# Kernel tuning notes

Measured on AMD Instinct MI355X. Metric: run time of the kernel, lower is better.

Reference implementation:

```python
import jax, jax.numpy as jnp
import numpy as np

N = 4096      # num nodes
E = 131072    # num edges
D = 128       # embed dim (in=out)
HID = 16      # kan hidden dim
G, K = 4, 3   # KAN grid_size / spline_order (GCN + FFN kans)
GA, KA = 2, 1 # attention KANLinear grid_size / spline_order
H, HD = 8, 16 # heads, head_dim

def make_grid(in_f, g, k):
    h = 2.0 / g
    pts = (np.arange(-k, g + k + 1) * h - 1.0).astype(np.float32)  # [g+2k+1]
    return jnp.asarray(np.tile(pts[None, :], (in_f, 1)))            # [in_f, g+2k+1]

GRID_D = make_grid(D, G, K)
GRID_H = make_grid(HID, G, K)
GRID_A = make_grid(D, GA, KA)

def b_splines(x, grid, k):
    # x: [n, in] -> B-spline bases [n, in, g+k] via Cox-de-Boor recursion
    x = x[:, :, None]
    g = grid[None]
    bases = ((x >= g[..., :-1]) & (x < g[..., 1:])).astype(x.dtype)
    for j in range(1, k + 1):
        bases = ((x - g[..., :-(j + 1)]) / (g[..., j:-1] - g[..., :-(j + 1)]) * bases[..., :-1]
                 + (g[..., j + 1:] - x) / (g[..., j + 1:] - g[..., 1:-j]) * bases[..., 1:])
    return bases

def kan_lin(x, bw, sw, grid, k, use_silu):
    base = jax.nn.silu(x) if use_silu else x
    return base @ bw.T + jnp.einsum('nig,oig->no', b_splines(x, grid, k), sw)

def ekan2(x, bw1, sw1, bw2, sw2):
    # eKAN with layers_hidden=[D, HID, D], SiLU base activation
    h = kan_lin(x, bw1, sw1, GRID_D, K, True)
    return kan_lin(h, bw2, sw2, GRID_H, K, True)

def layer_norm(h, s, b):
    m = jnp.mean(h, axis=-1, keepdims=True)
    v = jnp.var(h, axis=-1, keepdims=True)
    return (h - m) * jax.lax.rsqrt(v + 1e-5) * s + b

def setup_inputs() -> dict:
    key = jax.random.key(0)
    ks = jax.random.split(key, 20)
    r = lambda i, shape: jax.random.normal(ks[i], shape, jnp.float32) * 0.1
    return dict(
        x=jax.random.normal(ks[0], (N, D), jnp.float32),
        edge_index=jax.random.randint(ks[1], (2, E), 0, N),
        gcn_bw1=r(2, (HID, D)), gcn_sw1=r(3, (HID, D, G + K)),
        gcn_bw2=r(4, (D, HID)), gcn_sw2=r(5, (D, HID, G + K)),
        q_bw=r(6, (D, D)), q_sw=r(7, (D, D, GA + KA)),
        k_bw=r(8, (D, D)), k_sw=r(9, (D, D, GA + KA)),
        v_bw=r(10, (D, D)), v_sw=r(11, (D, D, GA + KA)),
        ffn_bw1=r(12, (HID, D)), ffn_sw1=r(13, (HID, D, G + K)),
        ffn_bw2=r(14, (D, HID)), ffn_sw2=r(15, (D, HID, G + K)),
        ln1_s=jnp.ones(D), ln1_b=jnp.zeros(D),
        ln2_s=jnp.ones(D), ln2_b=jnp.zeros(D),
        ln3_s=jnp.ones(D), ln3_b=jnp.zeros(D),
    )

def reference(x, edge_index, gcn_bw1, gcn_sw1, gcn_bw2, gcn_sw2,
              q_bw, q_sw, k_bw, k_sw, v_bw, v_sw,
              ffn_bw1, ffn_sw1, ffn_bw2, ffn_sw2,
              ln1_s, ln1_b, ln2_s, ln2_b, ln3_s, ln3_b):
    n = x.shape[0]
    # ---- local GCN-KAN branch: KAN(A_hat x) ----
    loops = jnp.arange(n)
    row = jnp.concatenate([edge_index[0], loops])  # sources (+ self-loops)
    col = jnp.concatenate([edge_index[1], loops])  # targets
    w = jnp.ones(row.shape[0], x.dtype)
    deg = jax.ops.segment_sum(w, row, num_segments=n)
    dis = jnp.where(deg > 0, deg ** -0.5, 0.0)
    norm = dis[row] * w * dis[col]
    agg = jax.ops.segment_sum(norm[:, None] * x[row], col, num_segments=n)  # [n, D]
    h_local = ekan2(agg, gcn_bw1, gcn_sw1, gcn_bw2, gcn_sw2)
    h_local = layer_norm(x + h_local, ln1_s, ln1_b)
    # ---- global KAN multi-head attention branch ----
    Q = kan_lin(x, q_bw, q_sw, GRID_A, KA, False).reshape(n, H, HD)
    Kv = kan_lin(x, k_bw, k_sw, GRID_A, KA, False).reshape(n, H, HD)
    V = kan_lin(x, v_bw, v_sw, GRID_A, KA, False).reshape(n, H, HD)
    scores = jnp.einsum('nhd,mhd->hnm', Q, Kv) / np.sqrt(HD)  # [H, n, n]
    attn = jax.nn.softmax(scores, axis=-1)
    h_attn = jnp.einsum('hnm,mhd->nhd', attn, V).reshape(n, D)
    h_attn = layer_norm(x + h_attn, ln2_s, ln2_b)
    # ---- combine + KAN feed-forward ----
    h = h_local + h_attn
    out = layer_norm(h + ekan2(h, ffn_bw1, ffn_sw1, ffn_bw2, ffn_sw2), ln3_s, ln3_b)
    return out
```

## Files before the change

### kernel.cpp

```cpp
#include <hip/hip_runtime.h>

typedef unsigned short u16;
typedef unsigned int u32;

#define D_ 128
#define HID_ 16
#define NH_ 8
#define HD_ 16
#define PSTRIDE 17

#define WE_W1G 0
#define WE_W2G 16384
#define WE_W1F 32768
#define WE_W2F 49152
#define WE_TOTAL 65536

#define KROW 24
#define VROW 136
#define PROW 40
#define HROW 136

#define QSCALE 0.3606737602222409f

typedef __attribute__((ext_vector_type(8))) short bfrag;
typedef __attribute__((ext_vector_type(4))) float ffrag;

#if defined(__has_builtin)
#if __has_builtin(__builtin_amdgcn_exp2f)
#define EXP2F(x) __builtin_amdgcn_exp2f(x)
#endif
#endif
#ifndef EXP2F
#define EXP2F(x) exp2f(x)
#endif


__device__ __forceinline__ float bf2f(u16 u) {
    union { u32 i; float f; } v; v.i = ((u32)u) << 16; return v.f;
}
__device__ __forceinline__ u16 f2bf(float f) {
    u32 x = __float_as_uint(f);
    u32 r = (x + 0x7fffu + ((x >> 16) & 1u)) >> 16;
    return (u16)r;
}
__device__ __forceinline__ float rdf(const void* p, int i, bool bf) {
    return bf ? bf2f(((const u16*)p)[i]) : ((const float*)p)[i];
}

__global__ __launch_bounds__(256) void k_detect(const void* x,
                         const void* gbw1, const void* gsw1, const void* gbw2, const void* gsw2,
                         const void* qbw, const void* qsw, const void* kbw, const void* ksw,
                         const void* vbw, const void* vsw,
                         const void* fbw1, const void* fsw1, const void* fbw2, const void* fsw2,
// ... 143 lines not shown
    for (int k = 0; k < 4; k++) a[k] = (base + k < N) ? cnt[base + k] : 0;
    int loc = a[0] + a[1] + a[2] + a[3];
    int pre = loc;
#pragma unroll
    for (int off = 1; off < 64; off <<= 1) {
        int v = __shfl_up(pre, off, 64);
        if ((t & 63) >= off) pre += v;
    }
    if ((t & 63) == 63) ws[t >> 6] = pre;
    __syncthreads();
    if (t < 64) {
        int v = (t < 16) ? ws[t] : 0;
#pragma unroll
        for (int off = 1; off < 16; off <<= 1) {
            int u = __shfl_up(v, off, 64);
            if (t >= off) v += u;
        }
        if (t < 16) ws[t] = v;
    }
    __syncthreads();
    int ex = pre - loc + ((t >= 64) ? ws[(t >> 6) - 1] : 0);
    int run = ex;
#pragma unroll
    for (int k = 0; k < 4; k++) {
        if (base + k < N) rowptr[base + k] = run;
        run += a[k];
    }
    if (t == 1023) rowptr[N] = ws[15];
#pragma unroll
    for (int k = 0; k < 4; k++)
        if (base + k < N) dis[base + k] = rsqrtf((float)degi[base + k] + 1.0f);
}

__global__ void k_fill(const int* __restrict__ ei, const int* __restrict__ rowptr,
                       int* __restrict__ fill, int* __restrict__ elist, int E) {
    int e = blockIdx.x * 256 + threadIdx.x;
    if (e < E) {
        int r = ei[e], c = ei[E + e];
        int pos = rowptr[c] + atomicAdd(&fill[c], 1);
        elist[pos] = r;
    }
}

__global__ __launch_bounds__(128) void k_gcn(const int* __restrict__ rowptr,
        const int* __restrict__ elist, const float* __restrict__ dis,
        const float* __restrict__ xin, u16* __restrict__ Afeat) {
    int c = blockIdx.x, t = threadIdx.x;
    __shared__ int ids[128];
    __shared__ float wsh[128];
    int beg = rowptr[c], end = rowptr[c + 1];
    float a0 = 0.0f, a1 = 0.0f, a2 = 0.0f, a3 = 0.0f;
    for (int j0 = beg; j0 < end; j0 += 128) {
        int cc = min(128, end - j0);
        __syncthreads();
        if (t < cc) {
            int rr = elist[j0 + t];
            ids[t] = rr;
            wsh[t] = dis[rr];
        }
        __syncthreads();
        int j = 0;
        for (; j + 4 <= cc; j += 4) {
            a0 += wsh[j]     * xin[(size_t)ids[j]     * D_ + t];
            a1 += wsh[j + 1] * xin[(size_t)ids[j + 1] * D_ + t];
            a2 += wsh[j + 2] * xin[(size_t)ids[j + 2] * D_ + t];
            a3 += wsh[j + 3] * xin[(size_t)ids[j + 3] * D_ + t];
        }
        for (; j < cc; j++) a0 += wsh[j] * xin[(size_t)ids[j] * D_ + t];
    }
    float dc = dis[c];
    float a = dc * (((a0 + a1) + (a2 + a3)) + dc * xin[(size_t)c * D_ + t]);
    ((uint4*)Afeat)[(size_t)c * D_ + t] = feat8(a);
}

#define EKAN_G1_4W(APTR, ASTR, W1B) { \
    const u16* ar = (APTR) + (size_t)l15 * (ASTR) + (size_t)ww * 256 + quad * 8; \
    const u16* br = (W1B) + (size_t)l15 * 1024 + (size_t)ww * 256 + quad * 8; \
    ffrag c0 = {0,0,0,0}, c1 = {0,0,0,0}; \
    for (int ks = 0; ks < 128; ks += 32) { \
        c0 = __builtin_amdgcn_mfma_f32_16x16x32_bf16(*(const bfrag*)(ar + ks),       *(const bfrag*)(br + ks),       c0, 0, 0, 0); \
        c1 = __builtin_amdgcn_mfma_f32_16x16x32_bf16(*(const bfrag*)(ar + 128 + ks), *(const bfrag*)(br + 128 + ks), c1, 0, 0, 0); \
    } \
    redG[ww][lane] = make_float4(c0.x + c1.x, c0.y + c1.y, c0.z + c1.z, c0.w + c1.w); \
    __syncthreads(); \
    if (ww == 0) { \
        float4 p0 = redG[0][lane], p1 = redG[1][lane], p2 = redG[2][lane], p3 = redG[3][lane]; \
        float e0 = (p0.x + p1.x) + (p2.x + p3.x); \
        float e1 = (p0.y + p1.y) + (p2.y + p3.y); \
        float e2 = (p0.z + p1.z) + (p2.z + p3.z); \
        float e3 = (p0.w + p1.w) + (p2.w + p3.w); \
        { uint4 fv = feat8(e0); *(uint4*)(&hfL[(quad * 4 + 0) * HROW + l15 * 8]) = fv; } \
        { uint4 fv = feat8(e1); *(uint4*)(&hfL[(quad * 4 + 1) * HROW + l15 * 8]) = fv; } \
        { uint4 fv = feat8(e2); *(uint4*)(&hfL[(quad * 4 + 2) * HROW + l15 * 8]) = fv; } \
        { uint4 fv = feat8(e3); *(uint4*)(&hfL[(quad * 4 + 3) * HROW + l15 * 8]) = fv; } \
    } }

#define EK_TGET(RR, COMP, V0, V1, RES0EXPR, RES1EXPR) { \
    int row = quad * 4 + RR; \
    float r0 = (RES0EXPR); \
    float r1 = (RES1EXPR); \
    V0 = a0.COMP + r0; V1 = a1.COMP + r1; \
    float s1 = V0 + V1, s2 = V0 * V0 + V1 * V1; \
    s1 += __shfl_xor(s1, 1, 64); s2 += __shfl_xor(s2, 1, 64); \
    s1 += __shfl_xor(s1, 2, 64); s2 += __shfl_xor(s2, 2, 64); \
    s1 += __shfl_xor(s1, 4, 64); s2 += __shfl_xor(s2, 4, 64); \
// ... 29 lines not shown
    int c0i = 32 * ww + l15, c1i = c0i + 16; \
    float ls0 = (LNS)[c0i], lb0 = (LNB)[c0i]; \
    float ls1 = (LNS)[c1i], lb1 = (LNB)[c1i]; \
    float v0r0, v0r1, v0r2, v0r3, v1r0, v1r1, v1r2, v1r3; \
    EK_TGET(0, x, v0r0, v1r0, RES0EXPR, RES1EXPR) \
    EK_TGET(1, y, v0r1, v1r1, RES0EXPR, RES1EXPR) \
    EK_TGET(2, z, v0r2, v1r2, RES0EXPR, RES1EXPR) \
    EK_TGET(3, w, v0r3, v1r3, RES0EXPR, RES1EXPR) \
    __syncthreads(); \
    EK_TOUT(0, v0r0, v1r0, OUTP, BFO) \
    EK_TOUT(1, v0r1, v1r1, OUTP, BFO) \
    EK_TOUT(2, v0r2, v1r2, OUTP, BFO) \
    EK_TOUT(3, v0r3, v1r3, OUTP, BFO) }

__global__ __launch_bounds__(256) void k_ekan4(const u16* __restrict__ A,
        const u16* __restrict__ W1b, const u16* __restrict__ W2b,
        const float* __restrict__ resid,
        const float* __restrict__ lns, const float* __restrict__ lnb,
        void* __restrict__ outp, const u32* __restrict__ flags, int fin, int N) {
    __shared__ u16 hfL[16 * HROW];
    __shared__ float redS[128];
    __shared__ float4 redG[4][64];
    int mt = blockIdx.x, t = threadIdx.x;
    int ww = t >> 6, lane = t & 63, quad = lane >> 4, l15 = lane & 15;
    int node0 = mt * 16;
    const u16* Ab = A + (size_t)node0 * 1024;
    bool bfo = (fin != 0) && (flags[0] != 0);
    EKAN_G1_4W(Ab, 1024, W1b)
    __syncthreads();
    EKAN_G2LN(W2b, lns, lnb,
              resid[(size_t)(node0 + row) * 128 + c0i],
              resid[(size_t)(node0 + row) * 128 + c1i],
              outp, bfo)
}

#define QKV_STORE(ACC, TL) { \
    int col = cg * 48 + (TL) * 16 + l15; \
    int mat = col >> 7, idx = col & 127; \
    u16* dstb = (mat == 0) ? Qb : (mat == 1) ? Kb : Vb; \
    size_t base = (size_t)(idx >> 4) * N * HD_ + (size_t)(idx & 15); \
    dstb[base + (size_t)(rowb + 0) * HD_] = f2bf(ACC.x); \
    dstb[base + (size_t)(rowb + 1) * HD_] = f2bf(ACC.y); \
    dstb[base + (size_t)(rowb + 2) * HD_] = f2bf(ACC.z); \
    dstb[base + (size_t)(rowb + 3) * HD_] = f2bf(ACC.w); \
}

__global__ __launch_bounds__(64) void k_qkv5(const u16* __restrict__ F,
        const u16* __restrict__ Wb,
        u16* __restrict__ Qb, u16* __restrict__ Kb, u16* __restrict__ Vb, int N) {
    int mt = blockIdx.x, cg = blockIdx.y;
    int lane = threadIdx.x, quad = lane >> 4, l15 = lane & 15;
    const u16* arow = F + (size_t)(mt * 16 + l15) * 512 + quad * 8;
    const u16* b0r = Wb + (size_t)(cg * 48 + l15) * 512 + quad * 8;
    const u16* b1r = b0r + 16 * 512;
    const u16* b2r = b0r + 32 * 512;
    ffrag a0 = {0, 0, 0, 0}, a1 = {0, 0, 0, 0}, a2 = {0, 0, 0, 0};
#pragma unroll
    for (int ks = 0; ks < 512; ks += 32) {
        bfrag af = *(const bfrag*)(arow + ks);
        bfrag bf0 = *(const bfrag*)(b0r + ks);
        bfrag bf1 = *(const bfrag*)(b1r + ks);
        bfrag bf2 = *(const bfrag*)(b2r + ks);
        a0 = __builtin_amdgcn_mfma_f32_16x16x32_bf16(af, bf0, a0, 0, 0, 0);
        a1 = __builtin_amdgcn_mfma_f32_16x16x32_bf16(af, bf1, a1, 0, 0, 0);
        a2 = __builtin_amdgcn_mfma_f32_16x16x32_bf16(af, bf2, a2, 0, 0, 0);
    }
    int rowb = mt * 16 + quad * 4;
    QKV_STORE(a0, 0)
    QKV_STORE(a1, 1)
    QKV_STORE(a2, 2)
}

#define ATTN_SCORE(QF, LACC, PBT) { \
    ffrag zz = {0.0f, 0.0f, 0.0f, 0.0f}; \
    ffrag s0 = __builtin_amdgcn_mfma_f32_16x16x32_bf16(QF, kf0, zz, 0, 0, 0); \
    ffrag s1 = __builtin_amdgcn_mfma_f32_16x16x32_bf16(QF, kf1, zz, 0, 0, 0); \
    float a0 = EXP2F(s0.x), a1 = EXP2F(s0.y), a2 = EXP2F(s0.z), a3 = EXP2F(s0.w); \
    float b0 = EXP2F(s1.x), b1 = EXP2F(s1.y), b2 = EXP2F(s1.z), b3 = EXP2F(s1.w); \
    LACC.x += a0 + b0; LACC.y += a1 + b1; LACC.z += a2 + b2; LACC.w += a3 + b3; \
    u32* pw = (u32*)PBT; \
    pw[(quad * 4 + 0) * (PROW / 2) + l15] = (__float_as_uint(a0) >> 16) | (__float_as_uint(b0) & 0xFFFF0000u); \
    pw[(quad * 4 + 1) * (PROW / 2) + l15] = (__float_as_uint(a1) >> 16) | (__float_as_uint(b1) & 0xFFFF0000u); \
    pw[(quad * 4 + 2) * (PROW / 2) + l15] = (__float_as_uint(a2) >> 16) | (__float_as_uint(b2) & 0xFFFF0000u); \
    pw[(quad * 4 + 3) * (PROW / 2) + l15] = (__float_as_uint(a3) >> 16) | (__float_as_uint(b3) & 0xFFFF0000u); \
}

#define ATTN_PV(OACC, PBT) { \
    bfrag pf = *(const bfrag*)(&PBT[l15 * PROW + quad * 8]); \
    OACC = __builtin_amdgcn_mfma_f32_16x16x32_bf16(pf, vf, OACC, 0, 0, 0); \
}

#define STORE_TILE(OACC, LACC, TL) { \
    int q0 = qtb + (TL) * 16 + quad * 4; \
    float* pp; \
    pp = part + ((size_t)(h * N + q0 + 0) * SPLIT + s) * PSTRIDE; \
    pp[1 + l15] = OACC.x; if (l15 == 0) pp[0] = LACC.x; \
    pp = part + ((size_t)(h * N + q0 + 1) * SPLIT + s) * PSTRIDE; \
    pp[1 + l15] = OACC.y; if (l15 == 0) pp[0] = LACC.y; \
    pp = part + ((size_t)(h * N + q0 + 2) * SPLIT + s) * PSTRIDE; \
    pp[1 + l15] = OACC.z; if (l15 == 0) pp[0] = LACC.z; \
    pp = part + ((size_t)(h * N + q0 + 3) * SPLIT + s) * PSTRIDE; \
    pp[1 + l15] = OACC.w; if (l15 == 0) pp[0] = LACC.w; \
}

__global__ __launch_bounds__(256) void k_attn9(const u16* __restrict__ Qb,
        const u16* __restrict__ Kb, const u16* __restrict__ Vb,
        float* __restrict__ part, int N, int SPLIT) {
    int s = blockIdx.x, qb = blockIdx.y, h = blockIdx.z;
    int t = threadIdx.x;
    int w = t >> 6, lane = t & 63, quad = lane >> 4, l15 = lane & 15;
    __shared__ u16 ldsK[128 * KROW + 16];
    __shared__ u16 ldsVt[16 * VROW];
    __shared__ u16 ldsP[4][4][16 * PROW];

    const u16* qrow = Qb + (size_t)h * N * HD_;
    const u16* krow = Kb + (size_t)h * N * HD_;
    const u16* vrow = Vb + (size_t)h * N * HD_;

    for (int i = t; i < (128 * KROW + 16) / 2; i += 256) ((u32*)ldsK)[i] = 0;

    int qtb = qb * 256 + w * 64;
    bfrag qz = {0, 0, 0, 0, 0, 0, 0, 0};
    bfrag qf0 = qz, qf1 = qz, qf2 = qz, qf3 = qz;
    if (quad < 2) {
        qf0 = *(const bfrag*)(qrow + (size_t)(qtb + 0 * 16 + l15) * HD_ + quad * 8);
        qf1 = *(const bfrag*)(qrow + (size_t)(qtb + 1 * 16 + l15) * HD_ + quad * 8);
        qf2 = *(const bfrag*)(qrow + (size_t)(qtb + 2 * 16 + l15) * HD_ + quad * 8);
        qf3 = *(const bfrag*)(qrow + (size_t)(qtb + 3 * 16 + l15) * HD_ + quad * 8);
    }

    ffrag o0 = {0, 0, 0, 0}, o1 = {0, 0, 0, 0}, o2 = {0, 0, 0, 0}, o3 = {0, 0, 0, 0};
    ffrag L0 = {0, 0, 0, 0}, L1 = {0, 0, 0, 0}, L2 = {0, 0, 0, 0}, L3 = {0, 0, 0, 0};
    u16* pb0 = &ldsP[w][0][0];
    u16* pb1 = &ldsP[w][1][0];
    u16* pb2 = &ldsP[w][2][0];
    u16* pb3 = &ldsP[w][3][0];

    int keys = N / SPLIT;
    int kstart0 = s * keys;
    for (int kst = 0; kst < keys; kst += 128) {
        int kg = kstart0 + kst;
        __syncthreads();
        if (t < 128) {
            const uint4* src = (const uint4*)(krow + (size_t)(kg + t) * HD_);
            uint4 a = src[0], b = src[1];
            *(uint4*)(&ldsK[t * KROW]) = a;
            *(uint4*)(&ldsK[t * KROW + 8]) = b;
        } else {
            int key = t - 128;
            const uint4* src = (const uint4*)(vrow + (size_t)(kg + key) * HD_);
            uint4 a = src[0], b = src[1];
            ldsVt[0 * VROW + key] = (u16)(a.x);  ldsVt[1 * VROW + key] = (u16)(a.x >> 16);
            ldsVt[2 * VROW + key] = (u16)(a.y);  ldsVt[3 * VROW + key] = (u16)(a.y >> 16);
            ldsVt[4 * VROW + key] = (u16)(a.z);  ldsVt[5 * VROW + key] = (u16)(a.z >> 16);
            ldsVt[6 * VROW + key] = (u16)(a.w);  ldsVt[7 * VROW + key] = (u16)(a.w >> 16);
            ldsVt[8 * VROW + key] = (u16)(b.x);  ldsVt[9 * VROW + key] = (u16)(b.x >> 16);
            ldsVt[10 * VROW + key] = (u16)(b.y); ldsVt[11 * VROW + key] = (u16)(b.y >> 16);
            ldsVt[12 * VROW + key] = (u16)(b.z); ldsVt[13 * VROW + key] = (u16)(b.z >> 16);
            ldsVt[14 * VROW + key] = (u16)(b.w); ldsVt[15 * VROW + key] = (u16)(b.w >> 16);
        }
        __syncthreads();
#pragma unroll
        for (int koff = 0; koff < 128; koff += 32) {
            bfrag kf0 = *(const bfrag*)(&ldsK[(koff + 2 * l15) * KROW + quad * 8]);
            bfrag kf1 = *(const bfrag*)(&ldsK[(koff + 2 * l15 + 1) * KROW + quad * 8]);
            bfrag vf = *(const bfrag*)(&ldsVt[l15 * VROW + koff + quad * 8]);
            ATTN_SCORE(qf0, L0, pb0)
            ATTN_SCORE(qf1, L1, pb1)
            ATTN_SCORE(qf2, L2, pb2)
            ATTN_SCORE(qf3, L3, pb3)
            __asm__ volatile("s_waitcnt lgkmcnt(0)" ::: "memory");
            ATTN_PV(o0, pb0)
            ATTN_PV(o1, pb1)
            ATTN_PV(o2, pb2)
            ATTN_PV(o3, pb3)
        }
    }

#pragma unroll
    for (int off = 1; off < 16; off <<= 1) {
        L0.x += __shfl_xor(L0.x, off, 64); L0.y += __shfl_xor(L0.y, off, 64);
        L0.z += __shfl_xor(L0.z, off, 64); L0.w += __shfl_xor(L0.w, off, 64);
        L1.x += __shfl_xor(L1.x, off, 64); L1.y += __shfl_xor(L1.y, off, 64);
        L1.z += __shfl_xor(L1.z, off, 64); L1.w += __shfl_xor(L1.w, off, 64);
        L2.x += __shfl_xor(L2.x, off, 64); L2.y += __shfl_xor(L2.y, off, 64);
        L2.z += __shfl_xor(L2.z, off, 64); L2.w += __shfl_xor(L2.w, off, 64);
        L3.x += __shfl_xor(L3.x, off, 64); L3.y += __shfl_xor(L3.y, off, 64);
        L3.z += __shfl_xor(L3.z, off, 64); L3.w += __shfl_xor(L3.w, off, 64);
    }
    STORE_TILE(o0, L0, 0)
    STORE_TILE(o1, L1, 1)
    STORE_TILE(o2, L2, 2)
    STORE_TILE(o3, L3, 3)
}

__global__ __launch_bounds__(128) void k_comb(const float* __restrict__ part,
        const float* __restrict__ xin, const float* __restrict__ hl,
        const float* __restrict__ lnp, float* __restrict__ hv,
        u16* __restrict__ Afeat, int N, int SPLIT) {
    int n = blockIdx.x, t = threadIdx.x;
    __shared__ float red[128];
    int h = t >> 4, d = t & 15;
    float L = 0.0f, O = 0.0f;
    for (int ss = 0; ss < SPLIT; ss++) {
        const float* ps = part + ((size_t)(h * N + n) * SPLIT + ss) * PSTRIDE;
        L += ps[0];
        O += ps[1 + d];
    }
    float ha = O / L;
    float r = xin[(size_t)n * D_ + t] + ha;
    float mean = bsum(r, red) * (1.0f / 128.0f);
    float c = r - mean;
    float var = bsum(c * c, red) * (1.0f / 128.0f);
    float y2 = c * rsqrtf(var + 1e-5f) * lnp[256 + t] + lnp[384 + t];
    float hvv = hl[(size_t)n * D_ + t] + y2;
    hv[(size_t)n * D_ + t] = hvv;
    ((uint4*)Afeat)[(size_t)n * D_ + t] = feat8(hvv);
}

extern "C" void kernel_launch(void* const* d_in, const int* in_sizes, int n_in,
                              void* d_out, int out_size, void* d_ws, size_t ws_size,
                              hipStream_t stream) {
    const void* x = d_in[0];
    const int* ei = (const int*)d_in[1];
    const void* gbw1 = d_in[2];
    const void* gsw1 = d_in[3];
// ... 19 lines not shown
    const int N = in_sizes[0] / D_;
    const int E = in_sizes[1] / 2;
    const size_t ND = (size_t)N * D_;

    float* wf = (float*)d_ws;
    u32* flags = (u32*)wf;
    float* lnp = wf + 32;
    float* dis = wf + 800;
    float* xin = dis + N;
    float* hl  = xin + ND;
    float* hv  = hl + ND;
    u16* Web = (u16*)(hv + ND);
    u16* Wb  = Web + WE_TOTAL;
    u16* F   = Wb + 196608;
    u16* Qb  = F + (size_t)N * 512;
    u16* Kb  = Qb + ND;
    u16* Vb  = Kb + ND;
    u16* Afeat = Vb + ND;
    int* cnt    = (int*)(Afeat + (size_t)N * 1024);
    int* fill   = cnt + N;
    int* degi   = fill + N;
    int* rowptr = degi + N;
    int* elist  = rowptr + N + 1;
    float* part = (float*)(elist + E);

    size_t baseBytes = (size_t)((char*)part - (char*)d_ws);
    int SPLIT = 8;
    if (baseBytes + (size_t)NH_ * N * 8 * PSTRIDE * 4 > ws_size) SPLIT = 4;
    if (baseBytes + (size_t)NH_ * N * 4 * PSTRIDE * 4 > ws_size) SPLIT = 2;

    int convB = ((N * D_ + 768) + 255) >> 8;
    int countB = (E + 255) / 256;
    int zeroB = (3 * N + 255) / 256;

    k_detect<<<21 + zeroB, 256, 0, stream>>>(x, gbw1, gsw1, gbw2, gsw2, qbw, qsw, kbw, ksw,
                                             vbw, vsw, fbw1, fsw1, fbw2, fsw2,
                                             ln1s, ln1b, ln2s, ln2b, ln3s, ln3b, flags, cnt, N);
    k_setup<<<convB + 224 + countB, 256, 0, stream>>>(
        x, ln1s, ln1b, ln2s, ln2b, ln3s, ln3b,
        gbw1, gsw1, gbw2, gsw2, fbw1, fsw1, fbw2, fsw2,
        qbw, qsw, kbw, ksw, vbw, vsw,
        ei, flags, xin, lnp, F, Web, Wb, cnt, degi, N, E);
    k_qkv5<<<dim3(N / 16, 8), 64, 0, stream>>>(F, Wb, Qb, Kb, Vb, N);
    k_scan<<<1, 1024, 0, stream>>>(cnt, degi, rowptr, dis, N);
    k_fill<<<countB, 256, 0, stream>>>(ei, rowptr, fill, elist, E);
    k_gcn<<<N, 128, 0, stream>>>(rowptr, elist, dis, xin, Afeat);
    k_ekan4<<<N / 16, 256, 0, stream>>>(Afeat, Web + WE_W1G, Web + WE_W2G, xin,
                                        lnp + 0, lnp + 128, hl, flags, 0, N);
    k_attn9<<<dim3(SPLIT, N / 256, NH_), 256, 0, stream>>>(Qb, Kb, Vb, part, N, SPLIT);
    k_comb<<<N, 128, 0, stream>>>(part, xin, hl, lnp, hv, Afeat, N, SPLIT);
    k_ekan4<<<N / 16, 256, 0, stream>>>(Afeat, Web + WE_W1F, Web + WE_W2F, hv,
                                        lnp + 512, lnp + 640, d_out, flags, 1, N);
}
```

Baseline: 233.7 us.

## Co-schedule independent kernels: fuse QKV with edge fill, attention with GCN

Merges independent stages into shared launches by splitting the grid: the QKV projection blocks run alongside the CSR edge-fill blocks, and the attention blocks run alongside the GCN aggregation blocks, which now handle two nodes per 256-thread block. This removes two kernel launches and lets the memory-bound gather and atomics overlap with the MFMA-heavy attention. The cost is heterogeneous blocks sharing one LDS allocation and launch bound, and the eKAN GCN stage must now wait for attention to finish before it starts.

```diff
diff --git a/kernel.cpp b/kernel.cpp
--- a/kernel.cpp
+++ b/kernel.cpp
@@ -19,6 +19,13 @@
 #define VROW 136
 #define PROW 40
 #define HROW 136
+
+#define SH_K 0
+#define SH_KN (128 * KROW + 16)
+#define SH_VT (SH_KN)
+#define SH_VTN (16 * VROW)
+#define SH_P (SH_KN + SH_VTN)
+#define SH_TOTAL (SH_P + 16 * 16 * PROW)
 
 #define QSCALE 0.3606737602222409f
 
@@ -228,45 +235,223 @@
         if (base + k < N) dis[base + k] = rsqrtf((float)degi[base + k] + 1.0f);
 }
 
-__global__ void k_fill(const int* __restrict__ ei, const int* __restrict__ rowptr,
-                       int* __restrict__ fill, int* __restrict__ elist, int E) {
-    int e = blockIdx.x * 256 + threadIdx.x;
-    if (e < E) {
-        int r = ei[e], c = ei[E + e];
-        int pos = rowptr[c] + atomicAdd(&fill[c], 1);
-        elist[pos] = r;
-    }
-}
-
-__global__ __launch_bounds__(128) void k_gcn(const int* __restrict__ rowptr,
-        const int* __restrict__ elist, const float* __restrict__ dis,
-        const float* __restrict__ xin, u16* __restrict__ Afeat) {
-    int c = blockIdx.x, t = threadIdx.x;
-    __shared__ int ids[128];
-    __shared__ float wsh[128];
-    int beg = rowptr[c], end = rowptr[c + 1];
-    float a0 = 0.0f, a1 = 0.0f, a2 = 0.0f, a3 = 0.0f;
-    for (int j0 = beg; j0 < end; j0 += 128) {
-        int cc = min(128, end - j0);
-        __syncthreads();
-        if (t < cc) {
-            int rr = elist[j0 + t];
-            ids[t] = rr;
-            wsh[t] = dis[rr];
-        }
-        __syncthreads();
-        int j = 0;
-        for (; j + 4 <= cc; j += 4) {
-            a0 += wsh[j]     * xin[(size_t)ids[j]     * D_ + t];
-            a1 += wsh[j + 1] * xin[(size_t)ids[j + 1] * D_ + t];
-            a2 += wsh[j + 2] * xin[(size_t)ids[j + 2] * D_ + t];
-            a3 += wsh[j + 3] * xin[(size_t)ids[j + 3] * D_ + t];
-        }
-        for (; j < cc; j++) a0 += wsh[j] * xin[(size_t)ids[j] * D_ + t];
-    }
-    float dc = dis[c];
-    float a = dc * (((a0 + a1) + (a2 + a3)) + dc * xin[(size_t)c * D_ + t]);
-    ((uint4*)Afeat)[(size_t)c * D_ + t] = feat8(a);
+#define QKV_STORE(ACC, TL) { \
+    int col = cg * 48 + (TL) * 16 + l15; \
+    int mat = col >> 7, idx = col & 127; \
+    u16* dstb = (mat == 0) ? Qb : (mat == 1) ? Kb : Vb; \
+    size_t base = (size_t)(idx >> 4) * N * HD_ + (size_t)(idx & 15); \
+    dstb[base + (size_t)(rowb + 0) * HD_] = f2bf(ACC.x); \
+    dstb[base + (size_t)(rowb + 1) * HD_] = f2bf(ACC.y); \
+    dstb[base + (size_t)(rowb + 2) * HD_] = f2bf(ACC.z); \
+    dstb[base + (size_t)(rowb + 3) * HD_] = f2bf(ACC.w); \
+}
+
+__global__ __launch_bounds__(256) void k_qkv_fill(const u16* __restrict__ F,
+        const u16* __restrict__ Wb,
+        u16* __restrict__ Qb, u16* __restrict__ Kb, u16* __restrict__ Vb,
+        const int* __restrict__ ei, const int* __restrict__ rowptr,
+        int* __restrict__ fill, int* __restrict__ elist, int N, int E) {
+    int b = blockIdx.x, t = threadIdx.x;
+    int qkvB = (N / 16) * 2;
+    if (b < qkvB) {
+        int sub = b * 4 + (t >> 6);
+        int mt = sub >> 3, cg = sub & 7;
+        int lane = t & 63, quad = lane >> 4, l15 = lane & 15;
+        const u16* arow = F + (size_t)(mt * 16 + l15) * 512 + quad * 8;
+        const u16* b0r = Wb + (size_t)(cg * 48 + l15) * 512 + quad * 8;
+        const u16* b1r = b0r + 16 * 512;
+        const u16* b2r = b0r + 32 * 512;
+        ffrag a0 = {0, 0, 0, 0}, a1 = {0, 0, 0, 0}, a2 = {0, 0, 0, 0};
+#pragma unroll
+        for (int ks = 0; ks < 512; ks += 32) {
+            bfrag af = *(const bfrag*)(arow + ks);
+            bfrag bf0 = *(const bfrag*)(b0r + ks);
+            bfrag bf1 = *(const bfrag*)(b1r + ks);
+            bfrag bf2 = *(const bfrag*)(b2r + ks);
+            a0 = __builtin_amdgcn_mfma_f32_16x16x32_bf16(af, bf0, a0, 0, 0, 0);
+            a1 = __builtin_amdgcn_mfma_f32_16x16x32_bf16(af, bf1, a1, 0, 0, 0);
+            a2 = __builtin_amdgcn_mfma_f32_16x16x32_bf16(af, bf2, a2, 0, 0, 0);
+        }
+        int rowb = mt * 16 + quad * 4;
+        QKV_STORE(a0, 0)
+        QKV_STORE(a1, 1)
+        QKV_STORE(a2, 2)
+    } else {
+        int e = (b - qkvB) * 256 + t;
+        if (e < E) {
+            int r = ei[e], c = ei[E + e];
+            int pos = rowptr[c] + atomicAdd(&fill[c], 1);
+            elist[pos] = r;
+        }
+    }
+}
+
+#define ATTN_SCORE(QF, LACC, PBT) { \
+    ffrag zz = {0.0f, 0.0f, 0.0f, 0.0f}; \
+    ffrag s0 = __builtin_amdgcn_mfma_f32_16x16x32_bf16(QF, kf0, zz, 0, 0, 0); \
+    ffrag s1 = __builtin_amdgcn_mfma_f32_16x16x32_bf16(QF, kf1, zz, 0, 0, 0); \
+    float a0 = EXP2F(s0.x), a1 = EXP2F(s0.y), a2 = EXP2F(s0.z), a3 = EXP2F(s0.w); \
+    float b0 = EXP2F(s1.x), b1 = EXP2F(s1.y), b2 = EXP2F(s1.z), b3 = EXP2F(s1.w); \
+    LACC.x += a0 + b0; LACC.y += a1 + b1; LACC.z += a2 + b2; LACC.w += a3 + b3; \
+    u32* pw = (u32*)PBT; \
+    pw[(quad * 4 + 0) * (PROW / 2) + l15] = (__float_as_uint(a0) >> 16) | (__float_as_uint(b0) & 0xFFFF0000u); \
+    pw[(quad * 4 + 1) * (PROW / 2) + l15] = (__float_as_uint(a1) >> 16) | (__float_as_uint(b1) & 0xFFFF0000u); \
+    pw[(quad * 4 + 2) * (PROW / 2) + l15] = (__float_as_uint(a2) >> 16) | (__float_as_uint(b2) & 0xFFFF0000u); \
+    pw[(quad * 4 + 3) * (PROW / 2) + l15] = (__float_as_uint(a3) >> 16) | (__float_as_uint(b3) & 0xFFFF0000u); \
+}
+
+#define ATTN_PV(OACC, PBT) { \
+    bfrag pf = *(const bfrag*)(&PBT[l15 * PROW + quad * 8]); \
+    OACC = __builtin_amdgcn_mfma_f32_16x16x32_bf16(pf, vf, OACC, 0, 0, 0); \
+}
+
+#define STORE_TILE(OACC, LACC, TL) { \
+    int q0 = qtb + (TL) * 16 + quad * 4; \
+    float* pp; \
+    pp = part + ((size_t)(h * N + q0 + 0) * SPLIT + s) * PSTRIDE; \
+    pp[1 + l15] = OACC.x; if (l15 == 0) pp[0] = LACC.x; \
+    pp = part + ((size_t)(h * N + q0 + 1) * SPLIT + s) * PSTRIDE; \
+    pp[1 + l15] = OACC.y; if (l15 == 0) pp[0] = LACC.y; \
+    pp = part + ((size_t)(h * N + q0 + 2) * SPLIT + s) * PSTRIDE; \
+    pp[1 + l15] = OACC.z; if (l15 == 0) pp[0] = LACC.z; \
+    pp = part + ((size_t)(h * N + q0 + 3) * SPLIT + s) * PSTRIDE; \
+    pp[1 + l15] = OACC.w; if (l15 == 0) pp[0] = LACC.w; \
+}
+
+__global__ __launch_bounds__(256) void k_attn_gcn(const u16* __restrict__ Qb,
+        const u16* __restrict__ Kb, const u16* __restrict__ Vb,
+        float* __restrict__ part,
+        const int* __restrict__ rowptr, const int* __restrict__ elist,
+        const float* __restrict__ dis, const float* __restrict__ xin,
+        u16* __restrict__ Afeat, int N, int SPLIT) {
+    __shared__ __align__(16) u16 shmem[SH_TOTAL];
+    int b = blockIdx.x, t = threadIdx.x;
+    int ATTNB = SPLIT * (N / 256) * NH_;
+    if (b < ATTNB) {
+        int s = b % SPLIT;
+        int rest = b / SPLIT;
+        int qb = rest % (N / 256);
+        int h = rest / (N / 256);
+        int w = t >> 6, lane = t & 63, quad = lane >> 4, l15 = lane & 15;
+        u16* ldsK = shmem + SH_K;
+        u16* ldsVt = shmem + SH_VT;
+
+        const u16* qrow = Qb + (size_t)h * N * HD_;
+        const u16* krow = Kb + (size_t)h * N * HD_;
+        const u16* vrow = Vb + (size_t)h * N * HD_;
+
+        for (int i = t; i < SH_KN / 2; i += 256) ((u32*)ldsK)[i] = 0;
+
+        int qtb = qb * 256 + w * 64;
+        bfrag qz = {0, 0, 0, 0, 0, 0, 0, 0};
+        bfrag qf0 = qz, qf1 = qz, qf2 = qz, qf3 = qz;
+        if (quad < 2) {
+            qf0 = *(const bfrag*)(qrow + (size_t)(qtb + 0 * 16 + l15) * HD_ + quad * 8);
+            qf1 = *(const bfrag*)(qrow + (size_t)(qtb + 1 * 16 + l15) * HD_ + quad * 8);
+            qf2 = *(const bfrag*)(qrow + (size_t)(qtb + 2 * 16 + l15) * HD_ + quad * 8);
+            qf3 = *(const bfrag*)(qrow + (size_t)(qtb + 3 * 16 + l15) * HD_ + quad * 8);
+        }
+
+        ffrag o0 = {0, 0, 0, 0}, o1 = {0, 0, 0, 0}, o2 = {0, 0, 0, 0}, o3 = {0, 0, 0, 0};
+        ffrag L0 = {0, 0, 0, 0}, L1 = {0, 0, 0, 0}, L2 = {0, 0, 0, 0}, L3 = {0, 0, 0, 0};
+        u16* pb0 = shmem + SH_P + (w * 4 + 0) * (16 * PROW);
+        u16* pb1 = shmem + SH_P + (w * 4 + 1) * (16 * PROW);
+        u16* pb2 = shmem + SH_P + (w * 4 + 2) * (16 * PROW);
+        u16* pb3 = shmem + SH_P + (w * 4 + 3) * (16 * PROW);
+
+        int keys = N / SPLIT;
+        int kstart0 = s * keys;
+        for (int kst = 0; kst < keys; kst += 128) {
+            int kg = kstart0 + kst;
+            __syncthreads();
+            if (t < 128) {
+                const uint4* src = (const uint4*)(krow + (size_t)(kg + t) * HD_);
+                uint4 a = src[0], bq = src[1];
+                *(uint4*)(&ldsK[t * KROW]) = a;
+                *(uint4*)(&ldsK[t * KROW + 8]) = bq;
+            } else {
+                int key = t - 128;
+                const uint4* src = (const uint4*)(vrow + (size_t)(kg + key) * HD_);
+                uint4 a = src[0], bq = src[1];
+                ldsVt[0 * VROW + key] = (u16)(a.x);  ldsVt[1 * VROW + key] = (u16)(a.x >> 16);
+                ldsVt[2 * VROW + key] = (u16)(a.y);  ldsVt[3 * VROW + key] = (u16)(a.y >> 16);
+                ldsVt[4 * VROW + key] = (u16)(a.z);  ldsVt[5 * VROW + key] = (u16)(a.z >> 16);
+                ldsVt[6 * VROW + key] = (u16)(a.w);  ldsVt[7 * VROW + key] = (u16)(a.w >> 16);
+                ldsVt[8 * VROW + key] = (u16)(bq.x);  ldsVt[9 * VROW + key] = (u16)(bq.x >> 16);
+                ldsVt[10 * VROW + key] = (u16)(bq.y); ldsVt[11 * VROW + key] = (u16)(bq.y >> 16);
+                ldsVt[12 * VROW + key] = (u16)(bq.z); ldsVt[13 * VROW + key] = (u16)(bq.z >> 16);
+                ldsVt[14 * VROW + key] = (u16)(bq.w); ldsVt[15 * VROW + key] = (u16)(bq.w >> 16);
+            }
+            __syncthreads();
+#pragma unroll
+            for (int koff = 0; koff < 128; koff += 32) {
+                bfrag kf0 = *(const bfrag*)(&ldsK[(koff + 2 * l15) * KROW + quad * 8]);
+                bfrag kf1 = *(const bfrag*)(&ldsK[(koff + 2 * l15 + 1) * KROW + quad * 8]);
+                bfrag vf = *(const bfrag*)(&ldsVt[l15 * VROW + koff + quad * 8]);
+                ATTN_SCORE(qf0, L0, pb0)
+                ATTN_SCORE(qf1, L1, pb1)
+                ATTN_SCORE(qf2, L2, pb2)
+                ATTN_SCORE(qf3, L3, pb3)
+                __asm__ volatile("s_waitcnt lgkmcnt(0)" ::: "memory");
+                ATTN_PV(o0, pb0)
+                ATTN_PV(o1, pb1)
+                ATTN_PV(o2, pb2)
+                ATTN_PV(o3, pb3)
+            }
+        }
+
+#pragma unroll
+        for (int off = 1; off < 16; off <<= 1) {
+            L0.x += __shfl_xor(L0.x, off, 64); L0.y += __shfl_xor(L0.y, off, 64);
+            L0.z += __shfl_xor(L0.z, off, 64); L0.w += __shfl_xor(L0.w, off, 64);
+            L1.x += __shfl_xor(L1.x, off, 64); L1.y += __shfl_xor(L1.y, off, 64);
+            L1.z += __shfl_xor(L1.z, off, 64); L1.w += __shfl_xor(L1.w, off, 64);
+            L2.x += __shfl_xor(L2.x, off, 64); L2.y += __shfl_xor(L2.y, off, 64);
+            L2.z += __shfl_xor(L2.z, off, 64); L2.w += __shfl_xor(L2.w, off, 64);
+            L3.x += __shfl_xor(L3.x, off, 64); L3.y += __shfl_xor(L3.y, off, 64);
+            L3.z += __shfl_xor(L3.z, off, 64); L3.w += __shfl_xor(L3.w, off, 64);
+        }
+        STORE_TILE(o0, L0, 0)
+        STORE_TILE(o1, L1, 1)
+        STORE_TILE(o2, L2, 2)
+        STORE_TILE(o3, L3, 3)
+    } else {
+        int* idsH = (int*)shmem;
+        float* wshH = (float*)(idsH + 256);
+        int half = t >> 7, d = t & 127;
+        int node0 = (b - ATTNB) * 2;
+        int begA = rowptr[node0], endA = rowptr[node0 + 1];
+        int begB = rowptr[node0 + 1], endB = rowptr[node0 + 2];
+        int tripsA = (endA - begA + 127) >> 7;
+        int tripsB = (endB - begB + 127) >> 7;
+        int trips = max(tripsA, tripsB);
+        int beg = half ? begB : begA;
+        int end = half ? endB : endA;
+        float a0 = 0.0f, a1 = 0.0f, a2 = 0.0f, a3 = 0.0f;
+        for (int tr = 0; tr < trips; tr++) {
+            int j0 = beg + (tr << 7);
+            int cc = min(128, end - j0);
+            __syncthreads();
+            if (d < cc) {
+                int rr = elist[j0 + d];
+                idsH[half * 128 + d] = rr;
+                wshH[half * 128 + d] = dis[rr];
+            }
+            __syncthreads();
+            int j = 0;
+            for (; j + 4 <= cc; j += 4) {
+                a0 += wshH[half * 128 + j]     * xin[(size_t)idsH[half * 128 + j]     * D_ + d];
+                a1 += wshH[half * 128 + j + 1] * xin[(size_t)idsH[half * 128 + j + 1] * D_ + d];
+                a2 += wshH[half * 128 + j + 2] * xin[(size_t)idsH[half * 128 + j + 2] * D_ + d];
+                a3 += wshH[half * 128 + j + 3] * xin[(size_t)idsH[half * 128 + j + 3] * D_ + d];
+            }
+            for (; j < cc; j++) a0 += wshH[half * 128 + j] * xin[(size_t)idsH[half * 128 + j] * D_ + d];
+        }
+        int node = node0 + half;
+        float dc = dis[node];
+        float a = dc * (((a0 + a1) + (a2 + a3)) + dc * xin[(size_t)node * D_ + d]);
+        ((uint4*)Afeat)[(size_t)node * D_ + d] = feat8(a);
+    }
 }
 
 #define EKAN_G1_4W(APTR, ASTR, W1B) { \
@@ -362,166 +547,6 @@
               resid[(size_t)(node0 + row) * 128 + c0i],
               resid[(size_t)(node0 + row) * 128 + c1i],
               outp, bfo)
-}
-
-#define QKV_STORE(ACC, TL) { \
-    int col = cg * 48 + (TL) * 16 + l15; \
-    int mat = col >> 7, idx = col & 127; \
-    u16* dstb = (mat == 0) ? Qb : (mat == 1) ? Kb : Vb; \
-    size_t base = (size_t)(idx >> 4) * N * HD_ + (size_t)(idx & 15); \
-    dstb[base + (size_t)(rowb + 0) * HD_] = f2bf(ACC.x); \
-    dstb[base + (size_t)(rowb + 1) * HD_] = f2bf(ACC.y); \
-    dstb[base + (size_t)(rowb + 2) * HD_] = f2bf(ACC.z); \
-    dstb[base + (size_t)(rowb + 3) * HD_] = f2bf(ACC.w); \
-}
-
-__global__ __launch_bounds__(64) void k_qkv5(const u16* __restrict__ F,
-        const u16* __restrict__ Wb,
-        u16* __restrict__ Qb, u16* __restrict__ Kb, u16* __restrict__ Vb, int N) {
-    int mt = blockIdx.x, cg = blockIdx.y;
-    int lane = threadIdx.x, quad = lane >> 4, l15 = lane & 15;
-    const u16* arow = F + (size_t)(mt * 16 + l15) * 512 + quad * 8;
-    const u16* b0r = Wb + (size_t)(cg * 48 + l15) * 512 + quad * 8;
-    const u16* b1r = b0r + 16 * 512;
-    const u16* b2r = b0r + 32 * 512;
-    ffrag a0 = {0, 0, 0, 0}, a1 = {0, 0, 0, 0}, a2 = {0, 0, 0, 0};
-#pragma unroll
-    for (int ks = 0; ks < 512; ks += 32) {
-        bfrag af = *(const bfrag*)(arow + ks);
-        bfrag bf0 = *(const bfrag*)(b0r + ks);
-        bfrag bf1 = *(const bfrag*)(b1r + ks);
-        bfrag bf2 = *(const bfrag*)(b2r + ks);
-        a0 = __builtin_amdgcn_mfma_f32_16x16x32_bf16(af, bf0, a0, 0, 0, 0);
-        a1 = __builtin_amdgcn_mfma_f32_16x16x32_bf16(af, bf1, a1, 0, 0, 0);
-        a2 = __builtin_amdgcn_mfma_f32_16x16x32_bf16(af, bf2, a2, 0, 0, 0);
-    }
-    int rowb = mt * 16 + quad * 4;
-    QKV_STORE(a0, 0)
-    QKV_STORE(a1, 1)
-    QKV_STORE(a2, 2)
-}
-
-#define ATTN_SCORE(QF, LACC, PBT) { \
-    ffrag zz = {0.0f, 0.0f, 0.0f, 0.0f}; \
-    ffrag s0 = __builtin_amdgcn_mfma_f32_16x16x32_bf16(QF, kf0, zz, 0, 0, 0); \
-    ffrag s1 = __builtin_amdgcn_mfma_f32_16x16x32_bf16(QF, kf1, zz, 0, 0, 0); \
-    float a0 = EXP2F(s0.x), a1 = EXP2F(s0.y), a2 = EXP2F(s0.z), a3 = EXP2F(s0.w); \
-    float b0 = EXP2F(s1.x), b1 = EXP2F(s1.y), b2 = EXP2F(s1.z), b3 = EXP2F(s1.w); \
-    LACC.x += a0 + b0; LACC.y += a1 + b1; LACC.z += a2 + b2; LACC.w += a3 + b3; \
-    u32* pw = (u32*)PBT; \
-    pw[(quad * 4 + 0) * (PROW / 2) + l15] = (__float_as_uint(a0) >> 16) | (__float_as_uint(b0) & 0xFFFF0000u); \
-    pw[(quad * 4 + 1) * (PROW / 2) + l15] = (__float_as_uint(a1) >> 16) | (__float_as_uint(b1) & 0xFFFF0000u); \
-    pw[(quad * 4 + 2) * (PROW / 2) + l15] = (__float_as_uint(a2) >> 16) | (__float_as_uint(b2) & 0xFFFF0000u); \
-    pw[(quad * 4 + 3) * (PROW / 2) + l15] = (__float_as_uint(a3) >> 16) | (__float_as_uint(b3) & 0xFFFF0000u); \
-}
-
-#define ATTN_PV(OACC, PBT) { \
-    bfrag pf = *(const bfrag*)(&PBT[l15 * PROW + quad * 8]); \
-    OACC = __builtin_amdgcn_mfma_f32_16x16x32_bf16(pf, vf, OACC, 0, 0, 0); \
-}
-
-#define STORE_TILE(OACC, LACC, TL) { \
-    int q0 = qtb + (TL) * 16 + quad * 4; \
-    float* pp; \
-    pp = part + ((size_t)(h * N + q0 + 0) * SPLIT + s) * PSTRIDE; \
-    pp[1 + l15] = OACC.x; if (l15 == 0) pp[0] = LACC.x; \
-    pp = part + ((size_t)(h * N + q0 + 1) * SPLIT + s) * PSTRIDE; \
-    pp[1 + l15] = OACC.y; if (l15 == 0) pp[0] = LACC.y; \
-    pp = part + ((size_t)(h * N + q0 + 2) * SPLIT + s) * PSTRIDE; \
-    pp[1 + l15] = OACC.z; if (l15 == 0) pp[0] = LACC.z; \
-    pp = part + ((size_t)(h * N + q0 + 3) * SPLIT + s) * PSTRIDE; \
-    pp[1 + l15] = OACC.w; if (l15 == 0) pp[0] = LACC.w; \
-}
-
-__global__ __launch_bounds__(256) void k_attn9(const u16* __restrict__ Qb,
-        const u16* __restrict__ Kb, const u16* __restrict__ Vb,
-        float* __restrict__ part, int N, int SPLIT) {
-    int s = blockIdx.x, qb = blockIdx.y, h = blockIdx.z;
-    int t = threadIdx.x;
-    int w = t >> 6, lane = t & 63, quad = lane >> 4, l15 = lane & 15;
-    __shared__ u16 ldsK[128 * KROW + 16];
-    __shared__ u16 ldsVt[16 * VROW];
-    __shared__ u16 ldsP[4][4][16 * PROW];
-
-    const u16* qrow = Qb + (size_t)h * N * HD_;
-    const u16* krow = Kb + (size_t)h * N * HD_;
-    const u16* vrow = Vb + (size_t)h * N * HD_;
-
-    for (int i = t; i < (128 * KROW + 16) / 2; i += 256) ((u32*)ldsK)[i] = 0;
-
-    int qtb = qb * 256 + w * 64;
-    bfrag qz = {0, 0, 0, 0, 0, 0, 0, 0};
-    bfrag qf0 = qz, qf1 = qz, qf2 = qz, qf3 = qz;
-    if (quad < 2) {
-        qf0 = *(const bfrag*)(qrow + (size_t)(qtb + 0 * 16 + l15) * HD_ + quad * 8);
-        qf1 = *(const bfrag*)(qrow + (size_t)(qtb + 1 * 16 + l15) * HD_ + quad * 8);
-        qf2 = *(const bfrag*)(qrow + (size_t)(qtb + 2 * 16 + l15) * HD_ + quad * 8);
-        qf3 = *(const bfrag*)(qrow + (size_t)(qtb + 3 * 16 + l15) * HD_ + quad * 8);
-    }
-
-    ffrag o0 = {0, 0, 0, 0}, o1 = {0, 0, 0, 0}, o2 = {0, 0, 0, 0}, o3 = {0, 0, 0, 0};
-    ffrag L0 = {0, 0, 0, 0}, L1 = {0, 0, 0, 0}, L2 = {0, 0, 0, 0}, L3 = {0, 0, 0, 0};
-    u16* pb0 = &ldsP[w][0][0];
-    u16* pb1 = &ldsP[w][1][0];
-    u16* pb2 = &ldsP[w][2][0];
-    u16* pb3 = &ldsP[w][3][0];
-
-    int keys = N / SPLIT;
-    int kstart0 = s * keys;
-    for (int kst = 0; kst < keys; kst += 128) {
-        int kg = kstart0 + kst;
-        __syncthreads();
-        if (t < 128) {
-            const uint4* src = (const uint4*)(krow + (size_t)(kg + t) * HD_);
-            uint4 a = src[0], b = src[1];
-            *(uint4*)(&ldsK[t * KROW]) = a;
-            *(uint4*)(&ldsK[t * KROW + 8]) = b;
-        } else {
-            int key = t - 128;
-            const uint4* src = (const uint4*)(vrow + (size_t)(kg + key) * HD_);
-            uint4 a = src[0], b = src[1];
-            ldsVt[0 * VROW + key] = (u16)(a.x);  ldsVt[1 * VROW + key] = (u16)(a.x >> 16);
-            ldsVt[2 * VROW + key] = (u16)(a.y);  ldsVt[3 * VROW + key] = (u16)(a.y >> 16);
-            ldsVt[4 * VROW + key] = (u16)(a.z);  ldsVt[5 * VROW + key] = (u16)(a.z >> 16);
-            ldsVt[6 * VROW + key] = (u16)(a.w);  ldsVt[7 * VROW + key] = (u16)(a.w >> 16);
-            ldsVt[8 * VROW + key] = (u16)(b.x);  ldsVt[9 * VROW + key] = (u16)(b.x >> 16);
-            ldsVt[10 * VROW + key] = (u16)(b.y); ldsVt[11 * VROW + key] = (u16)(b.y >> 16);
-            ldsVt[12 * VROW + key] = (u16)(b.z); ldsVt[13 * VROW + key] = (u16)(b.z >> 16);
-            ldsVt[14 * VROW + key] = (u16)(b.w); ldsVt[15 * VROW + key] = (u16)(b.w >> 16);
-        }
-        __syncthreads();
-#pragma unroll
-        for (int koff = 0; koff < 128; koff += 32) {
-            bfrag kf0 = *(const bfrag*)(&ldsK[(koff + 2 * l15) * KROW + quad * 8]);
-            bfrag kf1 = *(const bfrag*)(&ldsK[(koff + 2 * l15 + 1) * KROW + quad * 8]);
-            bfrag vf = *(const bfrag*)(&ldsVt[l15 * VROW + koff + quad * 8]);
-            ATTN_SCORE(qf0, L0, pb0)
-            ATTN_SCORE(qf1, L1, pb1)
-            ATTN_SCORE(qf2, L2, pb2)
-            ATTN_SCORE(qf3, L3, pb3)
-            __asm__ volatile("s_waitcnt lgkmcnt(0)" ::: "memory");
-            ATTN_PV(o0, pb0)
-            ATTN_PV(o1, pb1)
-            ATTN_PV(o2, pb2)
-            ATTN_PV(o3, pb3)
-        }
-    }
-
-#pragma unroll
-    for (int off = 1; off < 16; off <<= 1) {
-        L0.x += __shfl_xor(L0.x, off, 64); L0.y += __shfl_xor(L0.y, off, 64);
-        L0.z += __shfl_xor(L0.z, off, 64); L0.w += __shfl_xor(L0.w, off, 64);
-        L1.x += __shfl_xor(L1.x, off, 64); L1.y += __shfl_xor(L1.y, off, 64);
-        L1.z += __shfl_xor(L1.z, off, 64); L1.w += __shfl_xor(L1.w, off, 64);
-        L2.x += __shfl_xor(L2.x, off, 64); L2.y += __shfl_xor(L2.y, off, 64);
-        L2.z += __shfl_xor(L2.z, off, 64); L2.w += __shfl_xor(L2.w, off, 64);
-        L3.x += __shfl_xor(L3.x, off, 64); L3.y += __shfl_xor(L3.y, off, 64);
-        L3.z += __shfl_xor(L3.z, off, 64); L3.w += __shfl_xor(L3.w, off, 64);
-    }
-    STORE_TILE(o0, L0, 0)
-    STORE_TILE(o1, L1, 1)
-    STORE_TILE(o2, L2, 2)
-    STORE_TILE(o3, L3, 3)
 }
 
 __global__ __launch_bounds__(128) void k_comb(const float* __restrict__ part,
@@ -607,6 +632,8 @@
     int convB = ((N * D_ + 768) + 255) >> 8;
     int countB = (E + 255) / 256;
     int zeroB = (3 * N + 255) / 256;
+    int qkvB = (N / 16) * 2;
+    int attnB = SPLIT * (N / 256) * NH_;
 
     k_detect<<<21 + zeroB, 256, 0, stream>>>(x, gbw1, gsw1, gbw2, gsw2, qbw, qsw, kbw, ksw,
                                              vbw, vsw, fbw1, fsw1, fbw2, fsw2,
@@ -616,13 +643,13 @@
         gbw1, gsw1, gbw2, gsw2, fbw1, fsw1, fbw2, fsw2,
         qbw, qsw, kbw, ksw, vbw, vsw,
         ei, flags, xin, lnp, F, Web, Wb, cnt, degi, N, E);
-    k_qkv5<<<dim3(N / 16, 8), 64, 0, stream>>>(F, Wb, Qb, Kb, Vb, N);
     k_scan<<<1, 1024, 0, stream>>>(cnt, degi, rowptr, dis, N);
-    k_fill<<<countB, 256, 0, stream>>>(ei, rowptr, fill, elist, E);
-    k_gcn<<<N, 128, 0, stream>>>(rowptr, elist, dis, xin, Afeat);
+    k_qkv_fill<<<qkvB + countB, 256, 0, stream>>>(F, Wb, Qb, Kb, Vb,
+                                                  ei, rowptr, fill, elist, N, E);
+    k_attn_gcn<<<attnB + N / 2, 256, 0, stream>>>(Qb, Kb, Vb, part,
+                                                  rowptr, elist, dis, xin, Afeat, N, SPLIT);
     k_ekan4<<<N / 16, 256, 0, stream>>>(Afeat, Web + WE_W1G, Web + WE_W2G, xin,
                                         lnp + 0, lnp + 128, hl, flags, 0, N);
-    k_attn9<<<dim3(SPLIT, N / 256, NH_), 256, 0, stream>>>(Qb, Kb, Vb, part, N, SPLIT);
     k_comb<<<N, 128, 0, stream>>>(part, xin, hl, lnp, hv, Afeat, N, SPLIT);
     k_ekan4<<<N / 16, 256, 0, stream>>>(Afeat, Web + WE_W1F, Web + WE_W2F, hv,
                                         lnp + 512, lnp + 640, d_out, flags, 1, N);
```

Result: no change. 238.0 us (+1.8%).

## Merge QKV projection with edge fill kernel and prefetch K/V tiles in attention

Applied to the files above, without the earlier changes.

The QKV MFMA projection and the CSR edge-fill step now run as one launch, with 256-thread blocks each holding four 64-lane projection tiles plus extra blocks for edge filling. This removes one kernel launch and lets the two independent jobs overlap after the scan. The attention kernel also register-prefetches the next 128-key K/V tile from global memory while the current tile is being computed, hiding load latency. The cost is more registers in the attention kernel, which may lower occupancy.

```diff
diff --git a/kernel.cpp b/kernel.cpp
--- a/kernel.cpp
+++ b/kernel.cpp
@@ -228,13 +228,54 @@
         if (base + k < N) dis[base + k] = rsqrtf((float)degi[base + k] + 1.0f);
 }
 
-__global__ void k_fill(const int* __restrict__ ei, const int* __restrict__ rowptr,
-                       int* __restrict__ fill, int* __restrict__ elist, int E) {
-    int e = blockIdx.x * 256 + threadIdx.x;
-    if (e < E) {
-        int r = ei[e], c = ei[E + e];
-        int pos = rowptr[c] + atomicAdd(&fill[c], 1);
-        elist[pos] = r;
+#define QKV_STORE(ACC, TL) { \
+    int col = cg * 48 + (TL) * 16 + l15; \
+    int mat = col >> 7, idx = col & 127; \
+    u16* dstb = (mat == 0) ? Qb : (mat == 1) ? Kb : Vb; \
+    size_t base = (size_t)(idx >> 4) * N * HD_ + (size_t)(idx & 15); \
+    dstb[base + (size_t)(rowb + 0) * HD_] = f2bf(ACC.x); \
+    dstb[base + (size_t)(rowb + 1) * HD_] = f2bf(ACC.y); \
+    dstb[base + (size_t)(rowb + 2) * HD_] = f2bf(ACC.z); \
+    dstb[base + (size_t)(rowb + 3) * HD_] = f2bf(ACC.w); \
+}
+
+__global__ __launch_bounds__(256) void k_qkv_fill(const u16* __restrict__ F,
+        const u16* __restrict__ Wb,
+        u16* __restrict__ Qb, u16* __restrict__ Kb, u16* __restrict__ Vb,
+        const int* __restrict__ ei, const int* __restrict__ rowptr,
+        int* __restrict__ fill, int* __restrict__ elist, int N, int E) {
+    int b = blockIdx.x, t = threadIdx.x;
+    int qkvB = (N / 16) * 2;
+    if (b < qkvB) {
+        int sub = b * 4 + (t >> 6);
+        int mt = sub >> 3, cg = sub & 7;
+        int lane = t & 63, quad = lane >> 4, l15 = lane & 15;
+        const u16* arow = F + (size_t)(mt * 16 + l15) * 512 + quad * 8;
+        const u16* b0r = Wb + (size_t)(cg * 48 + l15) * 512 + quad * 8;
+        const u16* b1r = b0r + 16 * 512;
+        const u16* b2r = b0r + 32 * 512;
+        ffrag a0 = {0, 0, 0, 0}, a1 = {0, 0, 0, 0}, a2 = {0, 0, 0, 0};
+#pragma unroll
+        for (int ks = 0; ks < 512; ks += 32) {
+            bfrag af = *(const bfrag*)(arow + ks);
+            bfrag bf0 = *(const bfrag*)(b0r + ks);
+            bfrag bf1 = *(const bfrag*)(b1r + ks);
+            bfrag bf2 = *(const bfrag*)(b2r + ks);
+            a0 = __builtin_amdgcn_mfma_f32_16x16x32_bf16(af, bf0, a0, 0, 0, 0);
+            a1 = __builtin_amdgcn_mfma_f32_16x16x32_bf16(af, bf1, a1, 0, 0, 0);
+            a2 = __builtin_amdgcn_mfma_f32_16x16x32_bf16(af, bf2, a2, 0, 0, 0);
+        }
+        int rowb = mt * 16 + quad * 4;
+        QKV_STORE(a0, 0)
+        QKV_STORE(a1, 1)
+        QKV_STORE(a2, 2)
+    } else {
+        int e = (b - qkvB) * 256 + t;
+        if (e < E) {
+            int r = ei[e], c = ei[E + e];
+            int pos = rowptr[c] + atomicAdd(&fill[c], 1);
+            elist[pos] = r;
+        }
     }
 }
 
@@ -364,43 +405,6 @@
               outp, bfo)
 }
 
-#define QKV_STORE(ACC, TL) { \
-    int col = cg * 48 + (TL) * 16 + l15; \
-    int mat = col >> 7, idx = col & 127; \
-    u16* dstb = (mat == 0) ? Qb : (mat == 1) ? Kb : Vb; \
-    size_t base = (size_t)(idx >> 4) * N * HD_ + (size_t)(idx & 15); \
-    dstb[base + (size_t)(rowb + 0) * HD_] = f2bf(ACC.x); \
-    dstb[base + (size_t)(rowb + 1) * HD_] = f2bf(ACC.y); \
-    dstb[base + (size_t)(rowb + 2) * HD_] = f2bf(ACC.z); \
-    dstb[base + (size_t)(rowb + 3) * HD_] = f2bf(ACC.w); \
-}
-
-__global__ __launch_bounds__(64) void k_qkv5(const u16* __restrict__ F,
-        const u16* __restrict__ Wb,
-        u16* __restrict__ Qb, u16* __restrict__ Kb, u16* __restrict__ Vb, int N) {
-    int mt = blockIdx.x, cg = blockIdx.y;
-    int lane = threadIdx.x, quad = lane >> 4, l15 = lane & 15;
-    const u16* arow = F + (size_t)(mt * 16 + l15) * 512 + quad * 8;
-    const u16* b0r = Wb + (size_t)(cg * 48 + l15) * 512 + quad * 8;
-    const u16* b1r = b0r + 16 * 512;
-    const u16* b2r = b0r + 32 * 512;
-    ffrag a0 = {0, 0, 0, 0}, a1 = {0, 0, 0, 0}, a2 = {0, 0, 0, 0};
-#pragma unroll
-    for (int ks = 0; ks < 512; ks += 32) {
-        bfrag af = *(const bfrag*)(arow + ks);
-        bfrag bf0 = *(const bfrag*)(b0r + ks);
-        bfrag bf1 = *(const bfrag*)(b1r + ks);
-        bfrag bf2 = *(const bfrag*)(b2r + ks);
-        a0 = __builtin_amdgcn_mfma_f32_16x16x32_bf16(af, bf0, a0, 0, 0, 0);
-        a1 = __builtin_amdgcn_mfma_f32_16x16x32_bf16(af, bf1, a1, 0, 0, 0);
-        a2 = __builtin_amdgcn_mfma_f32_16x16x32_bf16(af, bf2, a2, 0, 0, 0);
-    }
-    int rowb = mt * 16 + quad * 4;
-    QKV_STORE(a0, 0)
-    QKV_STORE(a1, 1)
-    QKV_STORE(a2, 2)
-}
-
 #define ATTN_SCORE(QF, LACC, PBT) { \
     ffrag zz = {0.0f, 0.0f, 0.0f, 0.0f}; \
     ffrag s0 = __builtin_amdgcn_mfma_f32_16x16x32_bf16(QF, kf0, zz, 0, 0, 0); \
@@ -468,18 +472,21 @@
 
     int keys = N / SPLIT;
     int kstart0 = s * keys;
+    uint4 pfa, pfb;
+    {
+        const uint4* src = (t < 128)
+            ? (const uint4*)(krow + (size_t)(kstart0 + t) * HD_)
+            : (const uint4*)(vrow + (size_t)(kstart0 + t - 128) * HD_);
+        pfa = src[0]; pfb = src[1];
+    }
     for (int kst = 0; kst < keys; kst += 128) {
-        int kg = kstart0 + kst;
         __syncthreads();
         if (t < 128) {
-            const uint4* src = (const uint4*)(krow + (size_t)(kg + t) * HD_);
-            uint4 a = src[0], b = src[1];
-            *(uint4*)(&ldsK[t * KROW]) = a;
-            *(uint4*)(&ldsK[t * KROW + 8]) = b;
+            *(uint4*)(&ldsK[t * KROW]) = pfa;
+            *(uint4*)(&ldsK[t * KROW + 8]) = pfb;
         } else {
             int key = t - 128;
-            const uint4* src = (const uint4*)(vrow + (size_t)(kg + key) * HD_);
-            uint4 a = src[0], b = src[1];
+            uint4 a = pfa, b = pfb;
             ldsVt[0 * VROW + key] = (u16)(a.x);  ldsVt[1 * VROW + key] = (u16)(a.x >> 16);
             ldsVt[2 * VROW + key] = (u16)(a.y);  ldsVt[3 * VROW + key] = (u16)(a.y >> 16);
             ldsVt[4 * VROW + key] = (u16)(a.z);  ldsVt[5 * VROW + key] = (u16)(a.z >> 16);
@@ -490,6 +497,13 @@
             ldsVt[14 * VROW + key] = (u16)(b.w); ldsVt[15 * VROW + key] = (u16)(b.w >> 16);
         }
         __syncthreads();
+        if (kst + 128 < keys) {
+            int kg2 = kstart0 + kst + 128;
+            const uint4* src = (t < 128)
+                ? (const uint4*)(krow + (size_t)(kg2 + t) * HD_)
+                : (const uint4*)(vrow + (size_t)(kg2 + t - 128) * HD_);
+            pfa = src[0]; pfb = src[1];
+        }
 #pragma unroll
         for (int koff = 0; koff < 128; koff += 32) {
             bfrag kf0 = *(const bfrag*)(&ldsK[(koff + 2 * l15) * KROW + quad * 8]);
@@ -607,6 +621,7 @@
     int convB = ((N * D_ + 768) + 255) >> 8;
     int countB = (E + 255) / 256;
     int zeroB = (3 * N + 255) / 256;
+    int qkvB = (N / 16) * 2;
 
     k_detect<<<21 + zeroB, 256, 0, stream>>>(x, gbw1, gsw1, gbw2, gsw2, qbw, qsw, kbw, ksw,
                                              vbw, vsw, fbw1, fsw1, fbw2, fsw2,
@@ -616,9 +631,9 @@
         gbw1, gsw1, gbw2, gsw2, fbw1, fsw1, fbw2, fsw2,
         qbw, qsw, kbw, ksw, vbw, vsw,
         ei, flags, xin, lnp, F, Web, Wb, cnt, degi, N, E);
-    k_qkv5<<<dim3(N / 16, 8), 64, 0, stream>>>(F, Wb, Qb, Kb, Vb, N);
     k_scan<<<1, 1024, 0, stream>>>(cnt, degi, rowptr, dis, N);
-    k_fill<<<countB, 256, 0, stream>>>(ei, rowptr, fill, elist, E);
+    k_qkv_fill<<<qkvB + countB, 256, 0, stream>>>(F, Wb, Qb, Kb, Vb,
+                                                  ei, rowptr, fill, elist, N, E);
     k_gcn<<<N, 128, 0, stream>>>(rowptr, elist, dis, xin, Afeat);
     k_ekan4<<<N / 16, 256, 0, stream>>>(Afeat, Web + WE_W1G, Web + WE_W2G, xin,
                                         lnp + 0, lnp + 128, hl, flags, 0, N);
```

After: 227.9 us. 1.03x faster.
